# Kernel optimization log

Hardware: AMD Instinct MI355X
Metric: run time of the kernel (lower is better)

## Reference

```python
import jax, jax.numpy as jnp
import numpy as np

N, E, K, DEG = 150_000, 3_000_000, 4, 2
S = K * K  # 16 kernel weight matrices (kernel_size=4, dim=2)


def spline_coeffs(edge_attr):
    """Open quadratic B-spline basis, dim=2, kernel_size=4.
    Returns C [E, 16]: per-edge coefficient for each kernel weight index."""
    u = jnp.clip(edge_attr, 0.0, 1.0)
    v = u * (K - DEG)                      # [E,2], in [0, K-DEG]
    kv = jnp.floor(v)
    t = v - kv                             # [E,2] fractional part
    # quadratic uniform B-spline pieces
    b = jnp.stack([0.5 * (1.0 - t) ** 2,
                   -t * t + t + 0.5,
                   0.5 * t * t], axis=-1)  # [E,2,3]
    idx = jnp.clip(kv[..., None].astype(jnp.int32) + jnp.arange(3), 0, K - 1)  # [E,2,3]
    basis = (b[:, 0, :, None] * b[:, 1, None, :]).reshape(-1, 9)               # [E,9]
    widx = (idx[:, 0, :, None] + K * idx[:, 1, None, :]).reshape(-1, 9)        # [E,9]
    e_ar = jnp.arange(widx.shape[0])[:, None]
    C = jnp.zeros((widx.shape[0], S), basis.dtype).at[e_ar, widx].add(basis)   # [E,16]
    return C


def spline_conv(x, src, dst, C, weight, root, bias):
    # out_i = sum_{e: dst=i} sum_k C[e,k] * x[src[e]] @ W[k]  + x_i @ root + bias
    x_j = x[src]                                              # [E, in] gather
    out = x @ root + bias                                     # root_weight + bias
    for k in range(S):  # static small loop over 16 kernel matrices
        agg = jax.ops.segment_sum(C[:, k:k + 1] * x_j, dst, num_segments=N)  # [N,in]
        out = out + agg @ weight[k]
    return out


def batch_norm(x, gamma, beta, eps=1e-5):
    m = x.mean(axis=0)
    v = x.var(axis=0)  # biased, as torch BatchNorm1d training forward
    return (x - m) * jax.lax.rsqrt(v + eps) * gamma + beta


def setup_inputs() -> dict:
    key = jax.random.key(0)
    ks = jax.random.split(key, 18)
    f32 = jnp.float32
    return {
        "x": jax.random.normal(ks[0], (N, 1), f32),
        "edge_index": jax.random.randint(ks[1], (2, E), 0, N),
        "edge_attr": jax.random.uniform(ks[2], (E, 2), f32),
        "w1": jax.random.normal(ks[3], (S, 1, 32), f32) * 0.25,
        "root1": jax.random.normal(ks[4], (1, 32), f32) * 0.25,
        "b1": jnp.zeros((32,), f32),
        "gamma1": jnp.ones((32,), f32),
        "beta1": jnp.zeros((32,), f32),
        "w2": jax.random.normal(ks[5], (S, 32, 64), f32) * 0.05,
        "root2": jax.random.normal(ks[6], (32, 64), f32) * 0.05,
        "b2": jnp.zeros((64,), f32),
        "gamma2": jnp.ones((64,), f32),
        "beta2": jnp.zeros((64,), f32),
        "fc1_w": jax.random.normal(ks[7], (64, 128), f32) * 0.1,
        "fc1_b": jnp.zeros((128,), f32),
        "fc2_w": jax.random.normal(ks[8], (128, 1), f32) * 0.1,
        "fc2_b": jnp.zeros((1,), f32),
    }


def reference(x, edge_index, edge_attr, w1, root1, b1, gamma1, beta1,
              w2, root2, b2, gamma2, beta2, fc1_w, fc1_b, fc2_w, fc2_b):
    src, dst = edge_index[0], edge_index[1]
    C = spline_coeffs(edge_attr)            # shared by both conv layers
    h = spline_conv(x, src, dst, C, w1, root1, b1)
    h = jax.nn.elu(batch_norm(h, gamma1, beta1))
    h = spline_conv(h, src, dst, C, w2, root2, b2)
    h = jax.nn.elu(batch_norm(h, gamma2, beta2))  # [N,64]; flatten is identity
    h = jax.nn.elu(h @ fc1_w + fc1_b)
    return h @ fc2_w + fc2_b                 # [N,1]
```

## Files before the change

kernel.cpp:

```cpp
#include <hip/hip_runtime.h>
#include <hip/hip_fp16.h>
#include <math.h>


typedef _Float16 half8 __attribute__((ext_vector_type(8)));
typedef _Float16 half4 __attribute__((ext_vector_type(4)));
typedef float    f32x4 __attribute__((ext_vector_type(4)));
typedef unsigned uintx2 __attribute__((ext_vector_type(2)));
typedef unsigned uintx4 __attribute__((ext_vector_type(4)));

#define ACHUNK 4096

__device__ __forceinline__ void bspline4(float a, float B[4]) {
    a = fminf(fmaxf(a, 0.f), 1.f);
    float v  = a * 2.0f;
    float kv = floorf(v);
    float t  = v - kv;
    int   ik = (int)kv;
    float b0 = 0.5f * (1.f - t) * (1.f - t);
    float b1 = (t - t * t) + 0.5f;
    float b2 = 0.5f * t * t;
    int c0 = ik;
    int c1 = ik + 1;
    int c2 = ik + 2; if (c2 > 3) c2 = 3;
#pragma unroll
    for (int j = 0; j < 4; ++j)
        B[j] = (c0 == j ? b0 : 0.f) + (c1 == j ? b1 : 0.f) + (c2 == j ? b2 : 0.f);
}

__device__ __forceinline__ float eluf(float x) {
    return x > 0.f ? x : expm1f(x);
}

__device__ __forceinline__ void unpack_basis(uint4 rec, float bu[4], float bv[4]) {
    float2 f01 = __half22float2(*(const __half2*)&rec.y);
    float2 f23 = __half22float2(*(const __half2*)&rec.z);
    float2 f45 = __half22float2(*(const __half2*)&rec.w);
    bu[0] = f01.x; bu[1] = f01.y; bu[2] = f23.x;
    bu[3] = 1.f - (bu[0] + bu[1] + bu[2]);
    bv[0] = f23.y; bv[1] = f45.x; bv[2] = f45.y;
    bv[3] = 1.f - (bv[0] + bv[1] + bv[2]);
}

__device__ __forceinline__ uint4 make_edge_rec(unsigned src, float u, float v) {
    float Bu[4], Bv[4];
    bspline4(u, Bu);
    bspline4(v, Bv);
    __half2 p01 = __floats2half2_rn(Bu[0], Bu[1]);
    __half2 p23 = __floats2half2_rn(Bu[2], Bv[0]);
    __half2 p45 = __floats2half2_rn(Bv[1], Bv[2]);
    uint4 rec;
    rec.x = src;
    rec.y = *(const unsigned*)&p01;
    rec.z = *(const unsigned*)&p23;
    rec.w = *(const unsigned*)&p45;
    return rec;
}


__global__ void kA1_hist(const int* __restrict__ dst, int E, int* __restrict__ cnt,
                         int nWG, int NBUK) {
    extern __shared__ int hist[];
    int wg = blockIdx.x, tid = threadIdx.x;
    for (int b = tid; b < NBUK; b += 256) hist[b] = 0;
    __syncthreads();
    int base = wg * ACHUNK;
    int end  = base + ACHUNK; if (end > E) end = E;
    for (int i = base + tid; i < end; i += 256)
        atomicAdd(&hist[dst[i] >> 8], 1);
    __syncthreads();
    for (int b = tid; b < NBUK; b += 256) cnt[b * nWG + wg] = hist[b];
}

__global__ void k_scan1(const int* __restrict__ in, int M,
                        int* __restrict__ outp, int* __restrict__ blockSums) {
    __shared__ int wsum[4];
    int tid  = threadIdx.x;
    int base = blockIdx.x * 1024 + tid * 4;
    int d0 = (base + 0) < M ? in[base + 0] : 0;
    int d1 = (base + 1) < M ? in[base + 1] : 0;
    int d2 = (base + 2) < M ? in[base + 2] : 0;
    int d3 = (base + 3) < M ? in[base + 3] : 0;
    int s4 = d0 + d1 + d2 + d3;
    int lane = tid & 63, wid = tid >> 6;
    int inc = s4;
#pragma unroll
    for (int off = 1; off < 64; off <<= 1) {
        int t = __shfl_up(inc, off);
        if (lane >= off) inc += t;
    }
    if (lane == 63) wsum[wid] = inc;
    __syncthreads();
    if (tid == 0) {
        int acc = 0;
#pragma unroll
        for (int w = 0; w < 4; ++w) { int t = wsum[w]; wsum[w] = acc; acc += t; }
    }
    __syncthreads();
    int ebase = wsum[wid] + inc - s4;
    if ((base + 0) < M) outp[base + 0] = ebase;
    if ((base + 1) < M) outp[base + 1] = ebase + d0;
    if ((base + 2) < M) outp[base + 2] = ebase + d0 + d1;
    if ((base + 3) < M) outp[base + 3] = ebase + d0 + d1 + d2;
    if (tid == 255) blockSums[blockIdx.x] = ebase + s4;
}

__global__ void k_scan2(const int* __restrict__ blockSums, int NB, int* __restrict__ blockOff) {
    __shared__ int sh[256];
    int tid = threadIdx.x;
    int i0 = 2 * tid, i1 = 2 * tid + 1;
    int a = (i0 < NB) ? blockSums[i0] : 0;
    int b = (i1 < NB) ? blockSums[i1] : 0;
    int p = a + b;
    sh[tid] = p;
    __syncthreads();
    for (int off = 1; off < 256; off <<= 1) {
        int v = (tid >= off) ? sh[tid - off] : 0;
        __syncthreads();
        sh[tid] += v;
        __syncthreads();
    }
    int excl = sh[tid] - p;
    if (i0 < NB) blockOff[i0] = excl;
    if (i1 < NB) blockOff[i1] = excl + a;
}

__global__ void k_scan3b(int* __restrict__ arr, const int* __restrict__ blockOff, int M) {
    int i = blockIdx.x * blockDim.x + threadIdx.x;
    if (i < M) arr[i] += blockOff[i >> 10];
}

__global__ __launch_bounds__(256) void kA2_fill(
    const int* __restrict__ ei, const float* __restrict__ attr, int E,
    const int* __restrict__ offs, int nWG, int NBUK,
    uint4* __restrict__ buf1, unsigned char* __restrict__ dl1) {
    extern __shared__ int lds[];
    int*      hist  = lds;
    int*      srcS  = hist + NBUK;
    unsigned* attrS = (unsigned*)(srcS + ACHUNK);
    unsigned* meta  = attrS + ACHUNK;
    __shared__ int wsum[4];
    int wg = blockIdx.x, tid = threadIdx.x;
    int base  = wg * ACHUNK;
    int csize = E - base; if (csize > ACHUNK) csize = ACHUNK;

    for (int b = tid; b < NBUK; b += 256) hist[b] = 0;
    __syncthreads();

    int dArr[16], ranks[16];
#pragma unroll
    for (int k = 0; k < 16; ++k) {
        int i = tid + (k << 8);
        if (i < csize) {
            int d = ei[E + base + i];
            dArr[k]  = d;
            ranks[k] = atomicAdd(&hist[d >> 8], 1);
        }
    }
    __syncthreads();

    int IT = (NBUK + 255) >> 8;
    int b0 = tid * IT;
    int lsum = 0;
    for (int k = 0; k < IT; ++k) {
        int b = b0 + k;
        if (b < NBUK) lsum += hist[b];
    }
    int lane = tid & 63, wid = tid >> 6;
    int inc = lsum;
#pragma unroll
    for (int off = 1; off < 64; off <<= 1) {
        int t = __shfl_up(inc, off);
        if (lane >= off) inc += t;
    }
    if (lane == 63) wsum[wid] = inc;
    __syncthreads();
    if (tid == 0) {
        int acc = 0;
#pragma unroll
        for (int w = 0; w < 4; ++w) { int t = wsum[w]; wsum[w] = acc; acc += t; }
    }
    __syncthreads();
    int run = wsum[wid] + inc - lsum;
    for (int k = 0; k < IT; ++k) {
        int b = b0 + k;
        if (b < NBUK) { int h = hist[b]; hist[b] = run; run += h; }
    }
    __syncthreads();

#pragma unroll
    for (int k = 0; k < 16; ++k) {
        int i = tid + (k << 8);
        if (i < csize) {
            int gi = base + i;
            int d  = dArr[k];
            int b  = d >> 8;
            int s  = hist[b] + ranks[k];
            meta[s] = (unsigned)i | ((unsigned)b << 12) | ((unsigned)(d & 255) << 22);
            srcS[i] = ei[gi];
            __half2 uv = __floats2half2_rn(attr[2 * gi], attr[2 * gi + 1]);
            attrS[i] = *(const unsigned*)&uv;
        }
    }
    __syncthreads();

    for (int s = tid; s < csize; s += 256) {
        unsigned mt = meta[s];
        int i = mt & 4095;
        int b = (mt >> 12) & 1023;
        unsigned av = attrS[i];
        float2 uv = __half22float2(*(const __half2*)&av);
        uint4 rec = make_edge_rec((unsigned)srcS[i], uv.x, uv.y);
        int gpos = offs[b * nWG + wg] + (s - hist[b]);
        buf1[gpos] = rec;
        dl1[gpos]  = (unsigned char)(mt >> 22);
    }
}


__global__ __launch_bounds__(256) void kB_sort(
    const uint4* __restrict__ buf1, const unsigned char* __restrict__ dl1,
    const int* __restrict__ off, int nWG, int NBUK, int N, int E,
    uint4* __restrict__ edges, int* __restrict__ rowptr) {
    __shared__ int hist[256], pref[256], curs[256];
    __shared__ int sbase, ssize;
    int b = blockIdx.x, tid = threadIdx.x;
    if (tid == 0) {
        int s  = off[b * nWG];
        int e2 = (b + 1 < NBUK) ? off[(b + 1) * nWG] : E;
        sbase = s; ssize = e2 - s;
    }
    hist[tid] = 0;
    __syncthreads();
    int base = sbase, size = ssize;
    for (int i = tid; i < size; i += 256) atomicAdd(&hist[dl1[base + i]], 1);
    __syncthreads();
    if (tid == 0) {
        int acc = 0;
        for (int j = 0; j < 256; ++j) { pref[j] = acc; acc += hist[j]; }
    }
    __syncthreads();
    curs[tid] = pref[tid];
    int node = b * 256 + tid;
    if (node < N) rowptr[node] = base + pref[tid];
    if (b == NBUK - 1 && tid == 0) rowptr[N] = E;
    __syncthreads();
    for (int i = tid; i < size; i += 256) {
        int p = atomicAdd(&curs[dl1[base + i]], 1);
        edges[base + p] = buf1[base + i];
    }
}


__global__ void k_w2pack(const float* __restrict__ w2, const float* __restrict__ root2,
                         _Float16* __restrict__ w2f) {
    int f = blockIdx.x * blockDim.x + threadIdx.x;
    int stride = gridDim.x * blockDim.x;
    for (; f < 34816; f += stride) {
        int j = f & 7, l = (f >> 3) & 63, t = (f >> 9) & 3;
        int o = t * 16 + (l & 15);
        float v;
        if (f < 32768) {
            int s  = f >> 11;
            int ch = ((l >> 4) << 3) + j;
            v = w2[(s * 32 + ch) * 64 + o];
        } else {
            int ci = ((l >> 4) << 3) + j;
            v = root2[ci * 64 + o];
        }
        w2f[f] = (_Float16)v;
    }
}


__global__ void k_fcpack(const float* __restrict__ fc1w, _Float16* __restrict__ fc1wf) {
    int f = blockIdx.x * blockDim.x + threadIdx.x;
    if (f >= 8192) return;
    int j = f & 7, l = (f >> 3) & 63, t = (f >> 9) & 7, s = f >> 12;
    int k = s * 32 + ((l >> 4) << 3) + j;
    int o = t * 16 + (l & 15);
    fc1wf[f] = (_Float16)fc1w[k * 128 + o];
}


__global__ void k_conv1(const float* __restrict__ x, const int* __restrict__ rowptr,
                        const uint4* __restrict__ edges,
                        const float* __restrict__ w1, const float* __restrict__ root1,
                        const float* __restrict__ b1, _Float16* __restrict__ h1h, int N) {
    __shared__ float w1s[16 * 32];
    __shared__ float r1s[32], b1s[32];
    int tid = threadIdx.x;
    for (int i = tid; i < 512; i += blockDim.x) w1s[i] = w1[i];
    if (tid < 32) { r1s[tid] = root1[tid]; b1s[tid] = b1[tid]; }
    __syncthreads();
    int n = blockIdx.x * blockDim.x + tid;
    if (n >= N) return;
    float agg[16] = {};
    int s = rowptr[n], e = rowptr[n + 1];

#define P1(rec, xs) { \
    float bu[4], bv[4]; \
    unpack_basis(rec, bu, bv); \
    float t0 = (xs) * bv[0], t1 = (xs) * bv[1], t2 = (xs) * bv[2], t3 = (xs) * bv[3]; \
    agg[0]  += bu[0] * t0; agg[1]  += bu[1] * t0; agg[2]  += bu[2] * t0; agg[3]  += bu[3] * t0; \
    agg[4]  += bu[0] * t1; agg[5]  += bu[1] * t1; agg[6]  += bu[2] * t1; agg[7]  += bu[3] * t1; \
    agg[8]  += bu[0] * t2; agg[9]  += bu[1] * t2; agg[10] += bu[2] * t2; agg[11] += bu[3] * t2; \
    agg[12] += bu[0] * t3; agg[13] += bu[1] * t3; agg[14] += bu[2] * t3; agg[15] += bu[3] * t3; }

    int j = s;
    for (; j + 3 < e; j += 4) {
        uint4 r0 = edges[j], r1 = edges[j + 1], r2 = edges[j + 2], r3 = edges[j + 3];
        float x0 = x[r0.x], x1 = x[r1.x], x2 = x[r2.x], x3 = x[r3.x];
        P1(r0, x0); P1(r1, x1); P1(r2, x2); P1(r3, x3);
    }
    for (; j < e; ++j) {
        uint4 r = edges[j];
        float xs = x[r.x];
        P1(r, xs);
    }
#undef P1

    float xn = x[n];
    _Float16* hp = h1h + (size_t)n * 32;
#pragma unroll
    for (int o8 = 0; o8 < 4; ++o8) {
        half8 hv;
#pragma unroll
        for (int oo = 0; oo < 8; ++oo) {
            int o = o8 * 8 + oo;
            float acc = b1s[o] + xn * r1s[o];
#pragma unroll
            for (int k = 0; k < 16; ++k) acc += agg[k] * w1s[k * 32 + o];
            hv[oo] = (_Float16)acc;
        }
        *(half8*)(hp + o8 * 8) = hv;
    }
}


template <int C>
__global__ void k_bnstath(const _Float16* __restrict__ h, int N, double* __restrict__ sums) {
    __shared__ float sh1[C], sh2[C];
    int tid  = blockIdx.x * blockDim.x + threadIdx.x;
    int c    = tid & (C - 1);
    int row  = tid / C;
    int rstr = (gridDim.x * blockDim.x) / C;
    float s1 = 0.f, s2 = 0.f;
    for (int r = row; r < N; r += rstr) {
        float v = (float)h[(size_t)r * C + c];
        s1 += v; s2 += v * v;
    }
    if (threadIdx.x < C) { sh1[threadIdx.x] = 0.f; sh2[threadIdx.x] = 0.f; }
    __syncthreads();
    atomicAdd(&sh1[c], s1);
    atomicAdd(&sh2[c], s2);
    __syncthreads();
    if (threadIdx.x < C) {
        atomicAdd(&sums[threadIdx.x],     (double)sh1[threadIdx.x]);
        atomicAdd(&sums[C + threadIdx.x], (double)sh2[threadIdx.x]);
    }
}

__global__ void k_bnfinal(const double* __restrict__ sums, const float* __restrict__ gamma,
                          const float* __restrict__ beta, int C, int N, float* __restrict__ scsh) {
    int c = threadIdx.x;
    if (c < C) {
        double m   = sums[c] / (double)N;
        double var = sums[C + c] / (double)N - m * m;
        float vpe  = (float)var + 1e-5f;
        float sc   = gamma[c] / sqrtf(vpe);
        scsh[c]     = sc;
        scsh[C + c] = beta[c] - (float)m * sc;
    }
}

__global__ void k_bnelu32h(_Float16* __restrict__ hh, int N, const float* __restrict__ scsh) {
    int total = N * 4;
    int i = blockIdx.x * blockDim.x + threadIdx.x;
    int stride = gridDim.x * blockDim.x;
    for (; i < total; i += stride) {
        half8 v = *(half8*)(hh + (size_t)i * 8);
        int c0 = (i * 8) & 31;
        half8 r;
#pragma unroll
        for (int j = 0; j < 8; ++j)
            r[j] = (_Float16)eluf((float)v[j] * scsh[c0 + j] + scsh[32 + c0 + j]);
        *(half8*)(hh + (size_t)i * 8) = r;
    }
}


__global__ __launch_bounds__(256) void k_ag2(
    const _Float16* __restrict__ h1h, const int* __restrict__ rowptr,
    const uint4* __restrict__ edges, const _Float16* __restrict__ w2f,
    const float* __restrict__ b2, _Float16* __restrict__ out2h, int N) {
    __shared__ __align__(16) unsigned aggW[16][262];
    __shared__ __align__(16) _Float16 basisL[4][16][76];
    __shared__ __align__(16) int      srcL[4][64];
    int tid = threadIdx.x, l = tid & 63, w = tid >> 6;
    int g = l >> 4, m = l & 15;
    int n0 = blockIdx.x * 16;
    const unsigned* h32 = (const unsigned*)h1h;

    for (int q = 0; q < 4; ++q) {
        int row = w * 4 + q;
        int n = n0 + row;
        if (n < N) {
            int s = __builtin_amdgcn_readfirstlane(rowptr[n]);
            int e = __builtin_amdgcn_readfirstlane(rowptr[n + 1]);
            f32x4 C0 = {0.f, 0.f, 0.f, 0.f}, C1 = C0;
            for (int t = s; t < e; t += 64) {
                int eg = t + l;
                bool act = eg < e;
                uint4 rec = edges[act ? eg : e - 1];
                srcL[w][l] = act ? (int)rec.x : 0;
                float bu[4], bv[4];
                unpack_basis(rec, bu, bv);
#pragma unroll
                for (int kv = 0; kv < 4; ++kv)
#pragma unroll
                    for (int ku = 0; ku < 4; ++ku)
                        basisL[w][kv * 4 + ku][l] = (_Float16)(bu[ku] * bv[kv]);
                int rem = e - t;
#pragma unroll
                for (int kh = 0; kh < 2; ++kh) {
                    if (kh == 1 && rem <= 32) break;
                    int ebase = kh * 32 + g * 8;
                    half4 alo = *(const half4*)&basisL[w][m][ebase];
                    half4 ahi = *(const half4*)&basisL[w][m][ebase + 4];
                    half8 a;
#pragma unroll
                    for (int i = 0; i < 4; ++i) { a[i] = alo[i]; a[4 + i] = ahi[i]; }
                    unsigned u[8];
#pragma unroll
                    for (int j = 0; j < 8; ++j) {
                        int sj = srcL[w][ebase + j];
                        bool aj = (t + ebase + j) < e;
                        unsigned uv = h32[(size_t)sj * 16 + m];
                        u[j] = aj ? uv : 0u;
                    }
                    uintx4 p0, p1;
#pragma unroll
                    for (int tt = 0; tt < 4; ++tt) {
                        p0[tt] = (u[2 * tt] & 0xFFFFu) | (u[2 * tt + 1] << 16);
                        p1[tt] = (u[2 * tt] >> 16) | (u[2 * tt + 1] & 0xFFFF0000u);
                    }
                    half8 b0 = __builtin_bit_cast(half8, p0);
                    half8 b1 = __builtin_bit_cast(half8, p1);
                    C0 = __builtin_amdgcn_mfma_f32_16x16x32_f16(a, b0, C0, 0, 0, 0);
                    C1 = __builtin_amdgcn_mfma_f32_16x16x32_f16(a, b1, C1, 0, 0, 0);
                }
            }
#pragma unroll
            for (int r = 0; r < 4; ++r) {
                __half2 hp = __floats2half2_rn(C0[r], C1[r]);
                aggW[row][(g * 4 + r) * 16 + m] = *(const unsigned*)&hp;
            }
        }
    }
    __syncthreads();

    f32x4 acc = {0.f, 0.f, 0.f, 0.f};
#pragma unroll
    for (int s = 0; s < 16; ++s) {
        uintx2 a01 = *(const uintx2*)&aggW[m][s * 16 + g * 4];
        uintx2 a23 = *(const uintx2*)&aggW[m][s * 16 + g * 4 + 2];
        uintx4 av; av[0] = a01[0]; av[1] = a01[1]; av[2] = a23[0]; av[3] = a23[1];
        half8 a = __builtin_bit_cast(half8, av);
        half8 b = *(const half8*)&w2f[(size_t)(((s * 4 + w) * 64) + l) * 8];
        acc = __builtin_amdgcn_mfma_f32_16x16x32_f16(a, b, acc, 0, 0, 0);
    }
    {
        int nn = n0 + m; if (nn > N - 1) nn = N - 1;
        half8 a = *(const half8*)&h1h[(size_t)nn * 32 + g * 8];
        half8 b = *(const half8*)&w2f[(size_t)(((64 + w) * 64) + l) * 8];
        acc = __builtin_amdgcn_mfma_f32_16x16x32_f16(a, b, acc, 0, 0, 0);
    }
    int o = w * 16 + m;
    float bb = b2[o];
#pragma unroll
    for (int r = 0; r < 4; ++r) {
        int node = n0 + g * 4 + r;
        if (node < N) out2h[(size_t)node * 64 + o] = (_Float16)(acc[r] + bb);
    }
}


__global__ __launch_bounds__(256) void k_fcm(
    const _Float16* __restrict__ out2h, const _Float16* __restrict__ fc1wf,
    const float* __restrict__ scsh, const float* __restrict__ fc1b,
    const float* __restrict__ fc2w, const float* __restrict__ fc2b,
    float* __restrict__ out, int N, int ntiles) {
    __shared__ _Float16 fw[8192];
    __shared__ float scs[64], shs[64], b1s[128], w2sv[128];
    int tid = threadIdx.x;
    {
        const uint4* s4 = (const uint4*)fc1wf;
        uint4* d4 = (uint4*)fw;
        for (int i = tid; i < 1024; i += 256) d4[i] = s4[i];
    }
    if (tid < 128) { b1s[tid] = fc1b[tid]; w2sv[tid] = fc2w[tid]; }
    if (tid < 64)  { scs[tid] = scsh[tid]; shs[tid] = scsh[64 + tid]; }
    __syncthreads();
    const half8* bp = (const half8*)fw;
    int l = tid & 63, w = tid >> 6;
    int g = l >> 4, m = l & 15, klo = g * 8;
    float f2b = fc2b[0];
    for (int tile = blockIdx.x * 4 + w; tile < ntiles; tile += gridDim.x * 4) {
        int base = tile * 16;
        int arow = base + m; if (arow > N - 1) arow = N - 1;
        const half8* hp = (const half8*)(out2h + (size_t)arow * 64 + klo);
        half8 r0 = hp[0];
        half8 r1 = hp[4];
        half8 a0, a1;
#pragma unroll
        for (int j = 0; j < 8; ++j) {
            int c0 = klo + j, c1 = 32 + klo + j;
            a0[j] = (_Float16)eluf((float)r0[j] * scs[c0] + shs[c0]);
            a1[j] = (_Float16)eluf((float)r1[j] * scs[c1] + shs[c1]);
        }
        f32x4 acc[8];
#pragma unroll
        for (int t = 0; t < 8; ++t) {
            f32x4 z = {0.f, 0.f, 0.f, 0.f};
            acc[t] = __builtin_amdgcn_mfma_f32_16x16x32_f16(a0, bp[t * 64 + l], z, 0, 0, 0);
            acc[t] = __builtin_amdgcn_mfma_f32_16x16x32_f16(a1, bp[(8 + t) * 64 + l], acc[t], 0, 0, 0);
        }
#pragma unroll
        for (int r = 0; r < 4; ++r) {
            float sum = 0.f;
#pragma unroll
            for (int t = 0; t < 8; ++t) {
                int o = t * 16 + m;
                sum += eluf(acc[t][r] + b1s[o]) * w2sv[o];
            }
            sum += __shfl_xor(sum, 1);
            sum += __shfl_xor(sum, 2);
            sum += __shfl_xor(sum, 4);
            sum += __shfl_xor(sum, 8);
            int node = base + g * 4 + r;
            if (m == 0 && node < N) out[node] = sum + f2b;
        }
    }
}


extern "C" void kernel_launch(void* const* d_in, const int* in_sizes, int n_in,
                              void* d_out, int out_size, void* d_ws, size_t ws_size,
                              hipStream_t stream) {
    const float* x     = (const float*)d_in[0];
    const int*   ei    = (const int*)  d_in[1];
    const float* attr  = (const float*)d_in[2];
    const float* w1    = (const float*)d_in[3];
    const float* root1 = (const float*)d_in[4];
    const float* b1    = (const float*)d_in[5];
    const float* g1    = (const float*)d_in[6];
    const float* be1   = (const float*)d_in[7];
    const float* w2    = (const float*)d_in[8];
    const float* root2 = (const float*)d_in[9];
    const float* b2    = (const float*)d_in[10];
    const float* g2    = (const float*)d_in[11];
    const float* be2   = (const float*)d_in[12];
    const float* fc1w  = (const float*)d_in[13];
    const float* fc1b  = (const float*)d_in[14];
    const float* fc2w  = (const float*)d_in[15];
    const float* fc2b  = (const float*)d_in[16];
    float* out = (float*)d_out;

    int N = in_sizes[0];
    int E = in_sizes[1] / 2;

    int nWG  = (E + ACHUNK - 1) / ACHUNK;
    int NBUK = (N + 255) >> 8;
    int M    = NBUK * nWG;

    char* ws = (char*)d_ws;
    size_t off = 0;
    auto alloc = [&](size_t bytes) -> void* {
        void* p = ws + off;
        off = (off + bytes + 255) & ~(size_t)255;
        return p;
    };
    int*      rowptr    = (int*)     alloc((size_t)(N + 1) * 4);
    int*      blockSums = (int*)     alloc(1024 * 4);
    int*      blockOff  = (int*)     alloc(1024 * 4);
    double*   bnsum1    = (double*)  alloc(128 * 8);
    double*   bnsum2    = (double*)  alloc(128 * 8);
    float*    scsh1     = (float*)   alloc(64 * 4);
    float*    scsh2     = (float*)   alloc(128 * 4);
    _Float16* w2f       = (_Float16*)alloc(34816 * 2);
    _Float16* fc1wf     = (_Float16*)alloc(8192 * 2);
    int*      cnt       = (int*)     alloc((size_t)M * 4);
    int*      offs      = (int*)     alloc((size_t)M * 4);
    uint4*    edges     = (uint4*)   alloc((size_t)E * 16);
    size_t    Roff      = off;
    _Float16* h1h       = (_Float16*)alloc((size_t)N * 32 * 2);
    _Float16* out2h     = (_Float16*)alloc((size_t)N * 64 * 2);
    uint4*         buf1 = (uint4*)(ws + Roff);
    unsigned char* dl1  = (unsigned char*)(ws + Roff + (size_t)E * 16);
    (void)n_in; (void)out_size; (void)ws_size;

    hipMemsetAsync(bnsum1, 0, 128 * 8, stream);
    hipMemsetAsync(bnsum2, 0, 128 * 8, stream);

    size_t ldsA1 = (size_t)NBUK * 4;
    size_t ldsA2 = (size_t)NBUK * 4 + (size_t)ACHUNK * 12;
    int NBs = (M + 1023) / 1024;

    k_w2pack<<<136, 256, 0, stream>>>(w2, root2, w2f);
    k_fcpack<<<32, 256, 0, stream>>>(fc1w, fc1wf);
    kA1_hist<<<nWG, 256, ldsA1, stream>>>(ei + E, E, cnt, nWG, NBUK);
    k_scan1<<<NBs, 256, 0, stream>>>(cnt, M, offs, blockSums);
    k_scan2<<<1, 256, 0, stream>>>(blockSums, NBs, blockOff);
    k_scan3b<<<(M + 255) / 256, 256, 0, stream>>>(offs, blockOff, M);
    kA2_fill<<<nWG, 256, ldsA2, stream>>>(ei, attr, E, offs, nWG, NBUK, buf1, dl1);
    kB_sort<<<NBUK, 256, 0, stream>>>(buf1, dl1, offs, nWG, NBUK, N, E, edges, rowptr);

    k_conv1<<<(N + 255) / 256, 256, 0, stream>>>(x, rowptr, edges, w1, root1, b1, h1h, N);
    k_bnstath<32><<<256, 256, 0, stream>>>(h1h, N, bnsum1);
    k_bnfinal<<<1, 64, 0, stream>>>(bnsum1, g1, be1, 32, N, scsh1);
    k_bnelu32h<<<1024, 256, 0, stream>>>(h1h, N, scsh1);

    k_ag2<<<(N + 15) / 16, 256, 0, stream>>>(h1h, rowptr, edges, w2f, b2, out2h, N);

    k_bnstath<64><<<256, 256, 0, stream>>>(out2h, N, bnsum2);
    k_bnfinal<<<1, 64, 0, stream>>>(bnsum2, g2, be2, 64, N, scsh2);

    int ntilesF = (N + 15) / 16;
    int gridF = (ntilesF + 3) / 4; if (gridF > 2344) gridF = 2344;
    k_fcm<<<gridF, 256, 0, stream>>>(out2h, fc1wf, scsh2, fc1b, fc2w, fc2b, out, N, ntilesF);
}
```

Before: 320.5 us.

## Shrink edge records to 8 bytes and recompute B-spline basis on the fly

Edge records go from 16 bytes (src plus six fp16 basis values) to 8 bytes: the raw fp16 (u,v) attributes, plus the 18-bit source index and the 8-bit local destination packed into one word. The separate per-edge destination byte array is dropped, and the sort kernel reads the local destination from the record. Conv kernels now recompute the quadratic B-spline basis from u,v in every layer, which cuts edge-stream traffic in the fill, sort and both aggregation passes at the cost of extra ALU work. The packing assumes source indices fit in 18 bits, which holds for N=150k.

Result: faster. 311.3 us (-2.9%).

```diff
diff --git a/kernel.cpp b/kernel.cpp
--- a/kernel.cpp
+++ b/kernel.cpp
@@ -32,29 +32,12 @@
     return x > 0.f ? x : expm1f(x);
 }
 
-__device__ __forceinline__ void unpack_basis(uint4 rec, float bu[4], float bv[4]) {
-    float2 f01 = __half22float2(*(const __half2*)&rec.y);
-    float2 f23 = __half22float2(*(const __half2*)&rec.z);
-    float2 f45 = __half22float2(*(const __half2*)&rec.w);
-    bu[0] = f01.x; bu[1] = f01.y; bu[2] = f23.x;
-    bu[3] = 1.f - (bu[0] + bu[1] + bu[2]);
-    bv[0] = f23.y; bv[1] = f45.x; bv[2] = f45.y;
-    bv[3] = 1.f - (bv[0] + bv[1] + bv[2]);
-}
-
-__device__ __forceinline__ uint4 make_edge_rec(unsigned src, float u, float v) {
-    float Bu[4], Bv[4];
-    bspline4(u, Bu);
-    bspline4(v, Bv);
-    __half2 p01 = __floats2half2_rn(Bu[0], Bu[1]);
-    __half2 p23 = __floats2half2_rn(Bu[2], Bv[0]);
-    __half2 p45 = __floats2half2_rn(Bv[1], Bv[2]);
-    uint4 rec;
-    rec.x = src;
-    rec.y = *(const unsigned*)&p01;
-    rec.z = *(const unsigned*)&p23;
-    rec.w = *(const unsigned*)&p45;
-    return rec;
+__device__ __forceinline__ void decode_edge8(uint2 rec, int& src,
+                                             float bu[4], float bv[4]) {
+    src = (int)(rec.x & 0u, rec.y & 0x3FFFFu);
+    float2 uv = __half22float2(*(const __half2*)&rec.x);
+    bspline4(uv.x, bu);
+    bspline4(uv.y, bv);
 }
 
 
@@ -133,11 +116,11 @@
 __global__ __launch_bounds__(256) void kA2_fill(
     const int* __restrict__ ei, const float* __restrict__ attr, int E,
     const int* __restrict__ offs, int nWG, int NBUK,
-    uint4* __restrict__ buf1, unsigned char* __restrict__ dl1) {
+    uint2* __restrict__ buf1) {
     extern __shared__ int lds[];
     int*      hist  = lds;
-    int*      srcS  = hist + NBUK;
-    unsigned* attrS = (unsigned*)(srcS + ACHUNK);
+    unsigned* recB  = (unsigned*)(hist + NBUK);
+    unsigned* attrS = recB + ACHUNK;
     unsigned* meta  = attrS + ACHUNK;
     __shared__ int wsum[4];
     int wg = blockIdx.x, tid = threadIdx.x;
@@ -196,8 +179,8 @@
             int d  = dArr[k];
             int b  = d >> 8;
             int s  = hist[b] + ranks[k];
-            meta[s] = (unsigned)i | ((unsigned)b << 12) | ((unsigned)(d & 255) << 22);
-            srcS[i] = ei[gi];
+            meta[s] = (unsigned)i | ((unsigned)b << 12);
+            recB[i] = (unsigned)ei[gi] | ((unsigned)(d & 255) << 18);
             __half2 uv = __floats2half2_rn(attr[2 * gi], attr[2 * gi + 1]);
             attrS[i] = *(const unsigned*)&uv;
         }
@@ -207,21 +190,20 @@
     for (int s = tid; s < csize; s += 256) {
         unsigned mt = meta[s];
         int i = mt & 4095;
-        int b = (mt >> 12) & 1023;
-        unsigned av = attrS[i];
-        float2 uv = __half22float2(*(const __half2*)&av);
-        uint4 rec = make_edge_rec((unsigned)srcS[i], uv.x, uv.y);
+        int b = mt >> 12;
+        uint2 rec;
+        rec.x = attrS[i];
+        rec.y = recB[i];
         int gpos = offs[b * nWG + wg] + (s - hist[b]);
         buf1[gpos] = rec;
-        dl1[gpos]  = (unsigned char)(mt >> 22);
     }
 }
 
 
 __global__ __launch_bounds__(256) void kB_sort(
-    const uint4* __restrict__ buf1, const unsigned char* __restrict__ dl1,
+    const uint2* __restrict__ buf1,
     const int* __restrict__ off, int nWG, int NBUK, int N, int E,
-    uint4* __restrict__ edges, int* __restrict__ rowptr) {
+    uint2* __restrict__ edges, int* __restrict__ rowptr) {
     __shared__ int hist[256], pref[256], curs[256];
     __shared__ int sbase, ssize;
     int b = blockIdx.x, tid = threadIdx.x;
@@ -233,7 +215,8 @@
     hist[tid] = 0;
     __syncthreads();
     int base = sbase, size = ssize;
-    for (int i = tid; i < size; i += 256) atomicAdd(&hist[dl1[base + i]], 1);
+    for (int i = tid; i < size; i += 256)
+        atomicAdd(&hist[(buf1[base + i].y >> 18) & 255], 1);
     __syncthreads();
     if (tid == 0) {
         int acc = 0;
@@ -246,8 +229,9 @@
     if (b == NBUK - 1 && tid == 0) rowptr[N] = E;
     __syncthreads();
     for (int i = tid; i < size; i += 256) {
-        int p = atomicAdd(&curs[dl1[base + i]], 1);
-        edges[base + p] = buf1[base + i];
+        uint2 rec = buf1[base + i];
+        int p = atomicAdd(&curs[(rec.y >> 18) & 255], 1);
+        edges[base + p] = rec;
     }
 }
 
@@ -284,7 +268,7 @@
 
 
 __global__ void k_conv1(const float* __restrict__ x, const int* __restrict__ rowptr,
-                        const uint4* __restrict__ edges,
+                        const uint2* __restrict__ edges,
                         const float* __restrict__ w1, const float* __restrict__ root1,
                         const float* __restrict__ b1, _Float16* __restrict__ h1h, int N) {
     __shared__ float w1s[16 * 32];
@@ -299,8 +283,9 @@
     int s = rowptr[n], e = rowptr[n + 1];
 
 #define P1(rec, xs) { \
+    float2 uv = __half22float2(*(const __half2*)&rec.x); \
     float bu[4], bv[4]; \
-    unpack_basis(rec, bu, bv); \
+    bspline4(uv.x, bu); bspline4(uv.y, bv); \
     float t0 = (xs) * bv[0], t1 = (xs) * bv[1], t2 = (xs) * bv[2], t3 = (xs) * bv[3]; \
     agg[0]  += bu[0] * t0; agg[1]  += bu[1] * t0; agg[2]  += bu[2] * t0; agg[3]  += bu[3] * t0; \
     agg[4]  += bu[0] * t1; agg[5]  += bu[1] * t1; agg[6]  += bu[2] * t1; agg[7]  += bu[3] * t1; \
@@ -309,13 +294,14 @@
 
     int j = s;
     for (; j + 3 < e; j += 4) {
-        uint4 r0 = edges[j], r1 = edges[j + 1], r2 = edges[j + 2], r3 = edges[j + 3];
-        float x0 = x[r0.x], x1 = x[r1.x], x2 = x[r2.x], x3 = x[r3.x];
+        uint2 r0 = edges[j], r1 = edges[j + 1], r2 = edges[j + 2], r3 = edges[j + 3];
+        float x0 = x[r0.y & 0x3FFFF], x1 = x[r1.y & 0x3FFFF];
+        float x2 = x[r2.y & 0x3FFFF], x3 = x[r3.y & 0x3FFFF];
         P1(r0, x0); P1(r1, x1); P1(r2, x2); P1(r3, x3);
     }
     for (; j < e; ++j) {
-        uint4 r = edges[j];
-        float xs = x[r.x];
+        uint2 r = edges[j];
+        float xs = x[r.y & 0x3FFFF];
         P1(r, xs);
     }
 #undef P1
@@ -392,7 +378,7 @@
 
 __global__ __launch_bounds__(256) void k_ag2(
     const _Float16* __restrict__ h1h, const int* __restrict__ rowptr,
-    const uint4* __restrict__ edges, const _Float16* __restrict__ w2f,
+    const uint2* __restrict__ edges, const _Float16* __restrict__ w2f,
     const float* __restrict__ b2, _Float16* __restrict__ out2h, int N) {
     __shared__ __align__(16) unsigned aggW[16][262];
     __shared__ __align__(16) _Float16 basisL[4][16][76];
@@ -412,10 +398,12 @@
             for (int t = s; t < e; t += 64) {
                 int eg = t + l;
                 bool act = eg < e;
-                uint4 rec = edges[act ? eg : e - 1];
-                srcL[w][l] = act ? (int)rec.x : 0;
+                uint2 rec = edges[act ? eg : e - 1];
+                srcL[w][l] = act ? (int)(rec.y & 0x3FFFFu) : 0;
+                float2 uvf = __half22float2(*(const __half2*)&rec.x);
                 float bu[4], bv[4];
-                unpack_basis(rec, bu, bv);
+                bspline4(uvf.x, bu);
+                bspline4(uvf.y, bv);
 #pragma unroll
                 for (int kv = 0; kv < 4; ++kv)
 #pragma unroll
@@ -592,12 +580,11 @@
     _Float16* fc1wf     = (_Float16*)alloc(8192 * 2);
     int*      cnt       = (int*)     alloc((size_t)M * 4);
     int*      offs      = (int*)     alloc((size_t)M * 4);
-    uint4*    edges     = (uint4*)   alloc((size_t)E * 16);
+    uint2*    edges     = (uint2*)   alloc((size_t)E * 8);
     size_t    Roff      = off;
     _Float16* h1h       = (_Float16*)alloc((size_t)N * 32 * 2);
     _Float16* out2h     = (_Float16*)alloc((size_t)N * 64 * 2);
-    uint4*         buf1 = (uint4*)(ws + Roff);
-    unsigned char* dl1  = (unsigned char*)(ws + Roff + (size_t)E * 16);
+    uint2* buf1 = (uint2*)(ws + Roff);
     (void)n_in; (void)out_size; (void)ws_size;
 
     hipMemsetAsync(bnsum1, 0, 128 * 8, stream);
@@ -613,8 +600,8 @@
     k_scan1<<<NBs, 256, 0, stream>>>(cnt, M, offs, blockSums);
     k_scan2<<<1, 256, 0, stream>>>(blockSums, NBs, blockOff);
     k_scan3b<<<(M + 255) / 256, 256, 0, stream>>>(offs, blockOff, M);
-    kA2_fill<<<nWG, 256, ldsA2, stream>>>(ei, attr, E, offs, nWG, NBUK, buf1, dl1);
-    kB_sort<<<NBUK, 256, 0, stream>>>(buf1, dl1, offs, nWG, NBUK, N, E, edges, rowptr);
+    kA2_fill<<<nWG, 256, ldsA2, stream>>>(ei, attr, E, offs, nWG, NBUK, buf1);
+    kB_sort<<<NBUK, 256, 0, stream>>>(buf1, offs, nWG, NBUK, N, E, edges, rowptr);
 
     k_conv1<<<(N + 255) / 256, 256, 0, stream>>>(x, rowptr, edges, w1, root1, b1, h1h, N);
     k_bnstath<32><<<256, 256, 0, stream>>>(h1h, N, bnsum1);
```
